# Performance work log

Measured on AMD Instinct MI355X. Metric: run time of the kernel, lower is better.

The kernel has to match this reference:

```python
import jax, jax.numpy as jnp
import numpy as np

B = 512          # number of drug-combination graphs (batch)
MAX_LEN = 128    # static padding for to_dense_batch
D_DRUG = 256     # drug_in_features (kdim = vdim)
D_CELL = 1024    # cell_in_features
H = 16           # nheads
HD = 64          # h (per-head dim)
E = H * HD       # embed_dim = 1024


def setup_inputs() -> dict:
    key = jax.random.key(0)
    ks = jax.random.split(key, 12)
    N = 32768
    x_nodes = jax.random.normal(ks[0], (N, D_DRUG), dtype=jnp.float32)
    guide = jnp.sort(jax.random.randint(ks[1], (N,), 0, B)).astype(jnp.int64)
    cell = jax.random.normal(ks[2], (B, D_CELL), dtype=jnp.float32)
    s = 0.02
    return {
        "x_nodes": x_nodes,
        "cell": cell,
        "Wq": jax.random.normal(ks[3], (E, E), dtype=jnp.float32) * s,
        "bq": jnp.zeros((E,), dtype=jnp.float32),
        "Wk": jax.random.normal(ks[4], (E, D_DRUG), dtype=jnp.float32) * s,
        "bk": jnp.zeros((E,), dtype=jnp.float32),
        "Wv": jax.random.normal(ks[5], (E, D_DRUG), dtype=jnp.float32) * s,
        "bv": jnp.zeros((E,), dtype=jnp.float32),
        "Wo": jax.random.normal(ks[6], (E, E), dtype=jnp.float32) * s,
        "bo": jnp.zeros((E,), dtype=jnp.float32),
        "Wc": jax.random.normal(ks[7], (E, D_CELL), dtype=jnp.float32) * s,
        "bc": jnp.zeros((E,), dtype=jnp.float32),
        "guide": guide,
    }


def _to_dense_batch(x_nodes, guide):
    # Faithful torch_geometric.to_dense_batch with static MAX_LEN padding.
    N = x_nodes.shape[0]
    ones = jnp.ones((N,), dtype=jnp.int32)
    counts = jax.ops.segment_sum(ones, guide, num_segments=B)      # [B]
    starts = jnp.cumsum(counts) - counts                            # [B]
    pos = jnp.arange(N, dtype=jnp.int32) - starts[guide]            # rank within segment
    dense = jnp.zeros((B, MAX_LEN, x_nodes.shape[1]), x_nodes.dtype).at[guide, pos].set(x_nodes)
    mask = jnp.zeros((B, MAX_LEN), dtype=bool).at[guide, pos].set(True)
    return dense, mask


def reference(x_nodes, cell, Wq, bq, Wk, bk, Wv, bv, Wo, bo, Wc, bc, guide):
    drug_key, mask = _to_dense_batch(x_nodes, guide)                # [B,M,D_DRUG], [B,M]
    # cell_query_fc then MHA q-projection (single query per graph)
    cq = cell @ Wc.T + bc                                           # [B,E]
    q = (cq @ Wq.T + bq).reshape(B, H, HD) * (HD ** -0.5)           # [B,H,hd]
    k = (drug_key @ Wk.T + bk).reshape(B, MAX_LEN, H, HD)           # [B,M,H,hd]
    v = (drug_key @ Wv.T + bv).reshape(B, MAX_LEN, H, HD)
    scores = jnp.einsum('bhd,bmhd->bhm', q, k)                      # [B,H,M]
    scores = jnp.where(mask[:, None, :], scores, -1e9)
    attn = jax.nn.softmax(scores, axis=-1)
    out = jnp.einsum('bhm,bmhd->bhd', attn, v).reshape(B, E)        # [B,E]
    out = out @ Wo.T + bo
    return jnp.concatenate([out, cell], axis=1)                     # [B, E + D_CELL]
```

## Files before the change

kernel.cpp:

```cpp
#include <hip/hip_runtime.h>
#include <hip/hip_bf16.h>
#include <math.h>

#define B_GRAPHS 512
#define MAXLEN   128
#define DDRUG    256
#define NH       16
#define EMB      1024

typedef __attribute__((ext_vector_type(4))) float f32x4;
typedef __attribute__((ext_vector_type(8))) short s16x8;
typedef __attribute__((ext_vector_type(4))) short s16x4;

__device__ inline short f2bf(float f) {
    unsigned u = __builtin_bit_cast(unsigned, f);
    u += 0x7FFF + ((u >> 16) & 1);
    return (short)(u >> 16);
}
__device__ inline float bf2f(short s) {
    unsigned u = ((unsigned)(unsigned short)s) << 16;
    return __builtin_bit_cast(float, u);
}

__device__ inline void gload16(const short* g, void* lds)
{
    __builtin_amdgcn_global_load_lds(
        (const __attribute__((address_space(1))) unsigned*)g,
        (__attribute__((address_space(3))) unsigned*)lds, 16, 0, 0);
}

__device__ inline void cvt4(const float* __restrict__ in, short* __restrict__ out, int j)
{
    f32x4 v = ((const f32x4*)in)[j];
    s16x4 o;
    o.x = f2bf(v.x); o.y = f2bf(v.y); o.z = f2bf(v.z); o.w = f2bf(v.w);
    ((s16x4*)out)[j] = o;
}

__global__ __launch_bounds__(256) void prep_kernel(
    const float* __restrict__ cell, const float* __restrict__ Wc,
    const float* __restrict__ Wq,   const float* __restrict__ Wo,
    const float* __restrict__ Wv,   const int* __restrict__ g32, int N,
    float* __restrict__ out, short* __restrict__ cell_bf, short* __restrict__ Wc_bf,
    short* __restrict__ Wq_bf, short* __restrict__ Wo_bf, short* __restrict__ Wv_bf,
    int* __restrict__ starts)
{
    const int stride = gridDim.x * 256;
    for (int i = blockIdx.x * 256 + threadIdx.x; i < 1114625; i += stride) {
        if      (i <  131072) cvt4(cell, cell_bf, i);
        else if (i <  393216) cvt4(Wc, Wc_bf, i - 131072);
        else if (i <  655360) cvt4(Wq, Wq_bf, i - 393216);
        else if (i <  917504) cvt4(Wo, Wo_bf, i - 655360);
        else if (i <  983040) cvt4(Wv, Wv_bf, i - 917504);
        else if (i < 1114112) {
            int j = i - 983040;
            int b = j >> 8, c4 = j & 255;
            *(f32x4*)&out[(size_t)b * 2048 + 1024 + c4 * 4] = ((const f32x4*)cell)[j];
        } else {
            int b = i - 1114112;
            bool is64 = (g32[N - 1] == 0);
            int lo = 0, hi = N;
            while (lo < hi) {
                int mid = (lo + hi) >> 1;
                int v = is64 ? g32[2 * mid] : g32[mid];
                if (v < b) lo = mid + 1; else hi = mid;
            }
            starts[b] = lo;
        }
    }
}

template<bool OUT_BF>
__global__ __launch_bounds__(256) void gemm32_bf16_nt(
    const short* __restrict__ A, int lda,
    const short* __restrict__ Bw, int ldb,
    const float* __restrict__ bias, void* __restrict__ Cout,
    int ldc, float scale, int K)
{
    __shared__ short As[32 * 64];
    __shared__ short Bs[32 * 64];
    const int t = threadIdx.x, lane = t & 63, w = t >> 6;
    const int wm = w >> 1, wn = w & 1;
    const int row0 = blockIdx.y * 32, col0 = blockIdx.x * 32;
    f32x4 c = {0.f, 0.f, 0.f, 0.f};

    const int blk = w * 64 + lane;
    const int r = blk >> 3, cp = blk & 7;
    const int gc = (cp ^ (r & 7)) * 8;
    const short* gA = &A [(size_t)(row0 + r) * lda + gc];
    const short* gB = &Bw[(size_t)(col0 + r) * ldb + gc];
    char* ldsA = (char*)As + w * 1024;
    char* ldsB = (char*)Bs + w * 1024;

    for (int kt = 0; kt < K; kt += 64) {
        gload16(gA + kt, ldsA);
        gload16(gB + kt, ldsB);
        __syncthreads();
        #pragma unroll
        for (int ks = 0; ks < 2; ++ks) {
            const int kk = (ks * 32 + (lane >> 4) * 8) * 2;
            int ra = wm * 16 + (lane & 15);
            s16x8 a = *(const s16x8*)((char*)As + ra * 128 + (kk ^ ((ra & 7) << 4)));
            int rb = wn * 16 + (lane & 15);
            s16x8 b = *(const s16x8*)((char*)Bs + rb * 128 + (kk ^ ((rb & 7) << 4)));
            c = __builtin_amdgcn_mfma_f32_16x16x32_bf16(a, b, c, 0, 0, 0);
        }
        __syncthreads();
    }
    const int m0 = row0 + wm * 16 + (lane >> 4) * 4;
    const int nn = col0 + wn * 16 + (lane & 15);
    #pragma unroll
    for (int r2 = 0; r2 < 4; ++r2) {
        float v = (c[r2] + bias[nn]) * scale;
        if (OUT_BF) ((short*)Cout)[(size_t)(m0 + r2) * ldc + nn] = f2bf(v);
        else        ((float*)Cout)[(size_t)(m0 + r2) * ldc + nn] = v;
    }
}

__global__ __launch_bounds__(256) void qk_kernel(
    const float* __restrict__ q, const float* __restrict__ Wk, short* __restrict__ qkout)
{
    __shared__ float q_s[8][64];
    const int bt = blockIdx.x, h = blockIdx.y, t = threadIdx.x;
    for (int i = t; i < 512; i += 256)
        q_s[i >> 6][i & 63] = q[(size_t)(bt * 8 + (i >> 6)) * EMB + h * 64 + (i & 63)];
    __syncthreads();
    float acc[8] = {};
    const float* wbase = &Wk[(size_t)h * 64 * DDRUG + t];
    #pragma unroll 4
    for (int j = 0; j < 64; ++j) {
        float wv = wbase[(size_t)j * DDRUG];
        #pragma unroll
        for (int bb = 0; bb < 8; ++bb) acc[bb] += q_s[bb][j] * wv;
    }
    #pragma unroll
    for (int bb = 0; bb < 8; ++bb)
        qkout[(size_t)(bt * 8 + bb) * 4096 + h * DDRUG + t] = f2bf(acc[bb]);
}

__global__ __launch_bounds__(256) void attn_kernel(
    const float* __restrict__ X, const short* __restrict__ qk,
    const int* __restrict__ starts, short* __restrict__ xbar, int Ntot)
{
    __shared__ short Xs[128 * 256];
    __shared__ float S_s[128 * 20];
    const int b = blockIdx.x, t = threadIdx.x;
    const int lane = t & 63, w = t >> 6;
    const int s0 = starts[b];
    int n = starts[b + 1] - s0;
    if (n > MAXLEN) n = MAXLEN;

    s16x8 af[8];
    {
        const short* qb = qk + (size_t)b * 4096 + (lane & 15) * 256 + (lane >> 4) * 8;
        #pragma unroll
        for (int ks = 0; ks < 8; ++ks) af[ks] = *(const s16x8*)(qb + ks * 32);
    }

    const int sr = t >> 2, scg = (t & 3) * 64;
    auto stageX = [&](int st) {
        int lrow = st * 64 + sr;
        int gm = s0 + lrow;
        if (gm > Ntot - 1) gm = Ntot - 1;
        const f32x4* src = (const f32x4*)(X + (size_t)gm * 256 + scg);
        int swzr = (sr & 7) << 4;
        #pragma unroll
        for (int j = 0; j < 8; ++j) {
            f32x4 a = src[2 * j], bb = src[2 * j + 1];
            s16x8 v;
            v[0] = f2bf(a.x);  v[1] = f2bf(a.y);  v[2] = f2bf(a.z);  v[3] = f2bf(a.w);
            v[4] = f2bf(bb.x); v[5] = f2bf(bb.y); v[6] = f2bf(bb.z); v[7] = f2bf(bb.w);
            *(s16x8*)((char*)Xs + lrow * 512 + (((scg + j * 8) * 2) ^ swzr)) = v;
        }
    };
    auto mfmaStage = [&](int st) {
        int lr = st * 64 + w * 16 + (lane & 15);
        int swzr = (lr & 7) << 4;
        f32x4 c = {0.f, 0.f, 0.f, 0.f};
        #pragma unroll
        for (int ks = 0; ks < 8; ++ks) {
            int k = ks * 32 + (lane >> 4) * 8;
            s16x8 bf = *(const s16x8*)((char*)Xs + lr * 512 + ((k * 2) ^ swzr));
            c = __builtin_amdgcn_mfma_f32_16x16x32_bf16(af[ks], bf, c, 0, 0, 0);
        }
        int hb = (lane >> 4) * 4;
        #pragma unroll
        for (int i = 0; i < 4; ++i) S_s[lr * 20 + hb + i] = c[i];
    };

    stageX(0);
    __syncthreads();
    if (n > 64) stageX(1);
    mfmaStage(0);
    if (n > 64) {
        __syncthreads();
        mfmaStage(1);
    }
    __syncthreads();

    #pragma unroll
    for (int hh = 0; hh < 4; ++hh) {
        int h = w * 4 + hh;
        float v0 = (lane < n)      ? S_s[lane * 20 + h]        : -INFINITY;
        float v1 = (lane + 64 < n) ? S_s[(lane + 64) * 20 + h] : -INFINITY;
        float mx = fmaxf(v0, v1);
        #pragma unroll
        for (int off = 32; off > 0; off >>= 1) mx = fmaxf(mx, __shfl_xor(mx, off, 64));
        float e0 = (lane < n)      ? __expf(v0 - mx) : 0.f;
        float e1 = (lane + 64 < n) ? __expf(v1 - mx) : 0.f;
        float sm = e0 + e1;
        #pragma unroll
        for (int off = 32; off > 0; off >>= 1) sm += __shfl_xor(sm, off, 64);
        float inv = 1.f / sm;
        if (lane < n)      S_s[lane * 20 + h]        = e0 * inv;
        if (lane + 64 < n) S_s[(lane + 64) * 20 + h] = e1 * inv;
    }
    __syncthreads();

    const int d = t;
    float acc[16] = {};
    #pragma unroll 2
    for (int m = 0; m < n; ++m) {
        float x = bf2f(*(const short*)((char*)Xs + m * 512 + ((2 * d) ^ ((m & 7) << 4))));
        const f32x4* prow = (const f32x4*)&S_s[m * 20];
        f32x4 p0 = prow[0], p1 = prow[1], p2 = prow[2], p3 = prow[3];
        acc[0]  += p0.x * x; acc[1]  += p0.y * x; acc[2]  += p0.z * x; acc[3]  += p0.w * x;
        acc[4]  += p1.x * x; acc[5]  += p1.y * x; acc[6]  += p1.z * x; acc[7]  += p1.w * x;
        acc[8]  += p2.x * x; acc[9]  += p2.y * x; acc[10] += p2.z * x; acc[11] += p2.w * x;
        acc[12] += p3.x * x; acc[13] += p3.y * x; acc[14] += p3.z * x; acc[15] += p3.w * x;
    }
    short* xb = xbar + (size_t)b * 4096 + d;
    #pragma unroll
    for (int h = 0; h < 16; ++h) xb[(size_t)h * 256] = f2bf(acc[h]);
}

__global__ __launch_bounds__(256) void outh_gemm(
    const short* __restrict__ xbar,
    const short* __restrict__ Wv_bf,
    const float* __restrict__ bv, short* __restrict__ outh)
{
    __shared__ short As[64 * 64];
    __shared__ short Bs[64 * 64];
    const int t = threadIdx.x, lane = t & 63, w = t >> 6;
    const int wm = w >> 1, wn = w & 1;
    const int h = blockIdx.y;
    const int row0 = blockIdx.x * 64;
    const short* A = xbar + (size_t)h * 256;
    const short* B = Wv_bf + (size_t)h * 64 * 256;
    f32x4 c[2][2] = {};

    const int sr = t >> 2, sc = (t & 3) * 16;
    const int swz = (sr & 7) << 4;
    const int kb0 = (lane >> 4) * 8;

    for (int kt = 0; kt < 256; kt += 64) {
        s16x8 va0 = *(const s16x8*)&A[(size_t)(row0 + sr) * 4096 + kt + sc];
        s16x8 va1 = *(const s16x8*)&A[(size_t)(row0 + sr) * 4096 + kt + sc + 8];
        s16x8 vb0 = *(const s16x8*)&B[(size_t)sr * 256 + kt + sc];
        s16x8 vb1 = *(const s16x8*)&B[(size_t)sr * 256 + kt + sc + 8];
        *(s16x8*)((char*)As + sr * 128 + ((sc * 2)      ^ swz)) = va0;
        *(s16x8*)((char*)As + sr * 128 + ((sc * 2 + 16) ^ swz)) = va1;
        *(s16x8*)((char*)Bs + sr * 128 + ((sc * 2)      ^ swz)) = vb0;
        *(s16x8*)((char*)Bs + sr * 128 + ((sc * 2 + 16) ^ swz)) = vb1;
        __syncthreads();
        #pragma unroll
        for (int ks = 0; ks < 2; ++ks) {
            const int kk = (ks * 32 + kb0) * 2;
            s16x8 a0, a1, b0, b1;
            {
                int r = wm * 32 + (lane & 15);
                a0 = *(const s16x8*)((char*)As + r * 128 + (kk ^ ((r & 7) << 4)));
                int r2 = r + 16;
                a1 = *(const s16x8*)((char*)As + r2 * 128 + (kk ^ ((r2 & 7) << 4)));
            }
            {
                int r = wn * 32 + (lane & 15);
                b0 = *(const s16x8*)((char*)Bs + r * 128 + (kk ^ ((r & 7) << 4)));
                int r2 = r + 16;
                b1 = *(const s16x8*)((char*)Bs + r2 * 128 + (kk ^ ((r2 & 7) << 4)));
            }
            c[0][0] = __builtin_amdgcn_mfma_f32_16x16x32_bf16(a0, b0, c[0][0], 0, 0, 0);
            c[0][1] = __builtin_amdgcn_mfma_f32_16x16x32_bf16(a0, b1, c[0][1], 0, 0, 0);
            c[1][0] = __builtin_amdgcn_mfma_f32_16x16x32_bf16(a1, b0, c[1][0], 0, 0, 0);
            c[1][1] = __builtin_amdgcn_mfma_f32_16x16x32_bf16(a1, b1, c[1][1], 0, 0, 0);
        }
        __syncthreads();
    }
    #pragma unroll
    for (int i = 0; i < 2; ++i)
    #pragma unroll
    for (int j = 0; j < 2; ++j) {
        int m0 = row0 + wm * 32 + i * 16 + (lane >> 4) * 4;
        int nn = wn * 32 + j * 16 + (lane & 15);
        #pragma unroll
        for (int r = 0; r < 4; ++r) {
            float v = c[i][j][r] + bv[h * 64 + nn];
            outh[(size_t)(m0 + r) * EMB + h * 64 + nn] = f2bf(v);
        }
    }
}

extern "C" void kernel_launch(void* const* d_in, const int* in_sizes, int n_in,
                              void* d_out, int out_size, void* d_ws, size_t ws_size,
                              hipStream_t stream)
{
    const float* x_nodes = (const float*)d_in[0];
    const float* cell    = (const float*)d_in[1];
    const float* Wq      = (const float*)d_in[2];
    const float* bq      = (const float*)d_in[3];
    const float* Wk      = (const float*)d_in[4];
    const float* Wv      = (const float*)d_in[6];
    const float* bv      = (const float*)d_in[7];
    const float* Wo      = (const float*)d_in[8];
    const float* bo      = (const float*)d_in[9];
    const float* Wc      = (const float*)d_in[10];
    const float* bc      = (const float*)d_in[11];
    const int*   guide   = (const int*)d_in[12];
    const int N = in_sizes[12];
    float* out = (float*)d_out;

    char* ws = (char*)d_ws;
    int*   starts  = (int*)ws;
    float* qf32    = (float*)(ws + 4096);
    short* cell_bf = (short*)(ws + 4096 + (2u << 20));
    short* cq_bf   = (short*)(ws + 4096 + (3u << 20));
    short* outh_bf = (short*)(ws + 4096 + (4u << 20));
    short* qk_bf   = (short*)(ws + 4096 + (5u << 20));
    short* xbar_bf = (short*)(ws + 4096 + (9u << 20));
    short* Wc_bf   = (short*)(ws + 4096 + (13u << 20));
    short* Wq_bf   = (short*)(ws + 4096 + (15u << 20));
    short* Wo_bf   = (short*)(ws + 4096 + (17u << 20));
    short* Wv_bf   = (short*)(ws + 4096 + (19u << 20));

    prep_kernel<<<2048, 256, 0, stream>>>(
        cell, Wc, Wq, Wo, Wv, guide, N, out,
        cell_bf, Wc_bf, Wq_bf, Wo_bf, Wv_bf, starts);

    gemm32_bf16_nt<true ><<<dim3(32, 16), 256, 0, stream>>>(
        cell_bf, 1024, Wc_bf, 1024, bc, cq_bf, 1024, 1.0f, 1024);
    gemm32_bf16_nt<false><<<dim3(32, 16), 256, 0, stream>>>(
        cq_bf, 1024, Wq_bf, 1024, bq, qf32, 1024, 0.125f, 1024);

    qk_kernel<<<dim3(B_GRAPHS / 8, NH), 256, 0, stream>>>(qf32, Wk, qk_bf);

    attn_kernel<<<B_GRAPHS, 256, 0, stream>>>(x_nodes, qk_bf, starts, xbar_bf, N);

    outh_gemm<<<dim3(8, NH), 256, 0, stream>>>(xbar_bf, Wv_bf, bv, outh_bf);

    gemm32_bf16_nt<false><<<dim3(32, 16), 256, 0, stream>>>(
        outh_bf, 1024, Wo_bf, 1024, bo, out, 2048, 1.0f, 1024);

    (void)in_sizes; (void)n_in; (void)out_size; (void)ws_size;
}
```

Before: 170.5 us.

## Double attention block size to 512 threads and split the weighted sum over rows

The attention kernel now runs 512 threads per graph. All 128 rows of X are staged in one pass, and each wave computes one 16-row score tile, so the two-stage staging loop goes away. The weighted sum over nodes is split between two halves of the block, with the partial sums combined through shared memory. This adds parallelism and removes a serialized stage per graph, in exchange for extra barriers, a shared-memory reduction, and possibly lower occupancy from the larger block. Rows beyond n are no longer loaded; the old code clamped their addresses and loaded them anyway.

```diff
diff --git a/kernel.cpp b/kernel.cpp
--- a/kernel.cpp
+++ b/kernel.cpp
@@ -138,7 +138,7 @@
         qkout[(size_t)(bt * 8 + bb) * 4096 + h * DDRUG + t] = f2bf(acc[bb]);
 }
 
-__global__ __launch_bounds__(256) void attn_kernel(
+__global__ __launch_bounds__(512) void attn_kernel(
     const float* __restrict__ X, const short* __restrict__ qk,
     const int* __restrict__ starts, short* __restrict__ xbar, int Ntot)
 {
@@ -157,24 +157,25 @@
         for (int ks = 0; ks < 8; ++ks) af[ks] = *(const s16x8*)(qb + ks * 32);
     }
 
-    const int sr = t >> 2, scg = (t & 3) * 64;
-    auto stageX = [&](int st) {
-        int lrow = st * 64 + sr;
-        int gm = s0 + lrow;
-        if (gm > Ntot - 1) gm = Ntot - 1;
-        const f32x4* src = (const f32x4*)(X + (size_t)gm * 256 + scg);
-        int swzr = (sr & 7) << 4;
-        #pragma unroll
-        for (int j = 0; j < 8; ++j) {
-            f32x4 a = src[2 * j], bb = src[2 * j + 1];
-            s16x8 v;
-            v[0] = f2bf(a.x);  v[1] = f2bf(a.y);  v[2] = f2bf(a.z);  v[3] = f2bf(a.w);
-            v[4] = f2bf(bb.x); v[5] = f2bf(bb.y); v[6] = f2bf(bb.z); v[7] = f2bf(bb.w);
-            *(s16x8*)((char*)Xs + lrow * 512 + (((scg + j * 8) * 2) ^ swzr)) = v;
-        }
-    };
-    auto mfmaStage = [&](int st) {
-        int lr = st * 64 + w * 16 + (lane & 15);
+    {
+        const int row = t >> 2, scg = (t & 3) * 64;
+        if (row < n) {
+            const f32x4* src = (const f32x4*)(X + (size_t)(s0 + row) * 256 + scg);
+            int swzr = (row & 7) << 4;
+            #pragma unroll
+            for (int j = 0; j < 8; ++j) {
+                f32x4 a = src[2 * j], bb = src[2 * j + 1];
+                s16x8 v;
+                v[0] = f2bf(a.x);  v[1] = f2bf(a.y);  v[2] = f2bf(a.z);  v[3] = f2bf(a.w);
+                v[4] = f2bf(bb.x); v[5] = f2bf(bb.y); v[6] = f2bf(bb.z); v[7] = f2bf(bb.w);
+                *(s16x8*)((char*)Xs + row * 512 + (((scg + j * 8) * 2) ^ swzr)) = v;
+            }
+        }
+    }
+    __syncthreads();
+
+    if (w * 16 < n) {
+        int lr = w * 16 + (lane & 15);
         int swzr = (lr & 7) << 4;
         f32x4 c = {0.f, 0.f, 0.f, 0.f};
         #pragma unroll
@@ -186,21 +187,12 @@
         int hb = (lane >> 4) * 4;
         #pragma unroll
         for (int i = 0; i < 4; ++i) S_s[lr * 20 + hb + i] = c[i];
-    };
-
-    stageX(0);
-    __syncthreads();
-    if (n > 64) stageX(1);
-    mfmaStage(0);
-    if (n > 64) {
-        __syncthreads();
-        mfmaStage(1);
-    }
-    __syncthreads();
-
-    #pragma unroll
-    for (int hh = 0; hh < 4; ++hh) {
-        int h = w * 4 + hh;
+    }
+    __syncthreads();
+
+    #pragma unroll
+    for (int hh = 0; hh < 2; ++hh) {
+        int h = w * 2 + hh;
         float v0 = (lane < n)      ? S_s[lane * 20 + h]        : -INFINITY;
         float v1 = (lane + 64 < n) ? S_s[(lane + 64) * 20 + h] : -INFINITY;
         float mx = fmaxf(v0, v1);
@@ -217,21 +209,34 @@
     }
     __syncthreads();
 
-    const int d = t;
+    const int d = t & 255, half = t >> 8;
     float acc[16] = {};
-    #pragma unroll 2
-    for (int m = 0; m < n; ++m) {
-        float x = bf2f(*(const short*)((char*)Xs + m * 512 + ((2 * d) ^ ((m & 7) << 4))));
-        const f32x4* prow = (const f32x4*)&S_s[m * 20];
-        f32x4 p0 = prow[0], p1 = prow[1], p2 = prow[2], p3 = prow[3];
-        acc[0]  += p0.x * x; acc[1]  += p0.y * x; acc[2]  += p0.z * x; acc[3]  += p0.w * x;
-        acc[4]  += p1.x * x; acc[5]  += p1.y * x; acc[6]  += p1.z * x; acc[7]  += p1.w * x;
-        acc[8]  += p2.x * x; acc[9]  += p2.y * x; acc[10] += p2.z * x; acc[11] += p2.w * x;
-        acc[12] += p3.x * x; acc[13] += p3.y * x; acc[14] += p3.z * x; acc[15] += p3.w * x;
-    }
-    short* xb = xbar + (size_t)b * 4096 + d;
-    #pragma unroll
-    for (int h = 0; h < 16; ++h) xb[(size_t)h * 256] = f2bf(acc[h]);
+    {
+        int mlo = half * 64;
+        int mhi = n < mlo + 64 ? n : mlo + 64;
+        for (int m = mlo; m < mhi; ++m) {
+            float x = bf2f(*(const short*)((char*)Xs + m * 512 + ((2 * d) ^ ((m & 7) << 4))));
+            const f32x4* prow = (const f32x4*)&S_s[m * 20];
+            f32x4 p0 = prow[0], p1 = prow[1], p2 = prow[2], p3 = prow[3];
+            acc[0]  += p0.x * x; acc[1]  += p0.y * x; acc[2]  += p0.z * x; acc[3]  += p0.w * x;
+            acc[4]  += p1.x * x; acc[5]  += p1.y * x; acc[6]  += p1.z * x; acc[7]  += p1.w * x;
+            acc[8]  += p2.x * x; acc[9]  += p2.y * x; acc[10] += p2.z * x; acc[11] += p2.w * x;
+            acc[12] += p3.x * x; acc[13] += p3.y * x; acc[14] += p3.z * x; acc[15] += p3.w * x;
+        }
+    }
+    __syncthreads();
+    float* pd = (float*)Xs;
+    if (half == 1) {
+        #pragma unroll
+        for (int h = 0; h < 16; ++h) pd[h * 256 + d] = acc[h];
+    }
+    __syncthreads();
+    if (half == 0) {
+        short* xb = xbar + (size_t)b * 4096 + d;
+        #pragma unroll
+        for (int h = 0; h < 16; ++h)
+            xb[(size_t)h * 256] = f2bf(acc[h] + pd[h * 256 + d]);
+    }
 }
 
 __global__ __launch_bounds__(256) void outh_gemm(
@@ -343,7 +348,7 @@
 
     qk_kernel<<<dim3(B_GRAPHS / 8, NH), 256, 0, stream>>>(qf32, Wk, qk_bf);
 
-    attn_kernel<<<B_GRAPHS, 256, 0, stream>>>(x_nodes, qk_bf, starts, xbar_bf, N);
+    attn_kernel<<<B_GRAPHS, 512, 0, stream>>>(x_nodes, qk_bf, starts, xbar_bf, N);
 
     outh_gemm<<<dim3(8, NH), 256, 0, stream>>>(xbar_bf, Wv_bf, bv, outh_bf);
 
```

Result: faster. 165.2 us (-3.1%).
